# Kernel tuning notes

Hardware: AMD Instinct MI355X
Metric: run time of the kernel (lower is better)

Reference implementation:

```python
import jax, jax.numpy as jnp
from jax import lax
import numpy as np

GRID = 256   # spatial_shape of the sparse voxel volume (D=H=W)
N_ACTIVE = 500000
K = 5        # kernel_size=5, padding=2, stride=1 -> 'same' box-sum conv


def setup_inputs() -> dict:
    key = jax.random.key(0)
    k1, k2 = jax.random.split(key)
    feats = jax.random.normal(k1, (N_ACTIVE,), dtype=jnp.float32)
    coords = jax.random.randint(k2, (N_ACTIVE, 3), 0, GRID, dtype=jnp.int32)
    return {"feats": feats, "coords": coords}


def reference(feats, coords):
    # Densify the sparse tensor: scatter active-voxel features into [B=1, C=1, D, H, W].
    vol = jnp.zeros((1, 1, GRID, GRID, GRID), dtype=feats.dtype)
    vol = vol.at[0, 0, coords[:, 0], coords[:, 1], coords[:, 2]].add(feats)
    # Frozen all-ones 5x5x5 kernel (weight.data = ones, requires_grad=False), no bias.
    kernel = jnp.ones((1, 1, K, K, K), dtype=feats.dtype)  # OIDHW
    pad = K // 2
    out = lax.conv_general_dilated(
        vol, kernel,
        window_strides=(1, 1, 1),
        padding=[(pad, pad)] * 3,
        dimension_numbers=("NCDHW", "OIDHW", "NCDHW"),
    )
    # Original returns a list of one dense volume; return the array.
    return out
```

## Files before the change

### kernel.cpp

```cpp
#include <hip/hip_runtime.h>

#define GRIDN 256
#define NVOX (GRIDN * GRIDN * GRIDN)

typedef float floatx4 __attribute__((ext_vector_type(4)));

__global__ __launch_bounds__(256) void k_prep(const int* __restrict__ coords,
                                              int* __restrict__ lin, int n) {
    int i = blockIdx.x * blockDim.x + threadIdx.x;
    if (i >= n) return;
    int d = coords[3 * i + 0];
    int h = coords[3 * i + 1];
    int w = coords[3 * i + 2];
    lin[i] = (d * GRIDN + h) * GRIDN + w;
}

__global__ __launch_bounds__(256) void k_zero4(floatx4* __restrict__ p, int n4) {
    int stride = gridDim.x * blockDim.x;
    floatx4 z = {0.f, 0.f, 0.f, 0.f};
    for (int i = blockIdx.x * blockDim.x + threadIdx.x; i < n4; i += stride)
        __builtin_nontemporal_store(z, &p[i]);
}

__global__ __launch_bounds__(256) void k_scatter(const float* __restrict__ feats,
                                                 const int* __restrict__ lin,
                                                 float* __restrict__ vol, int n) {
    int i = blockIdx.x * blockDim.x + threadIdx.x;
    if (i >= n) return;
    atomicAdd(&vol[lin[i]], feats[i]);
}

#define TXF 64
#define TYF 16
#define ZS  16
__global__ __launch_bounds__(256) void k_fused(const float4* __restrict__ in4,
                                               float* __restrict__ out) {
    __shared__ float R[TYF + 4][72];
    __shared__ float Xp[TYF + 4][64];

    const int tid = threadIdx.x;

    int wg  = blockIdx.x;
    int swz = (wg & 7) * 128 + (wg >> 3);
    const int x0 = (swz & 3) * TXF;
    const int y0 = ((swz >> 2) & 15) * TYF;
    const int z0 = (swz >> 6) * ZS;

    const int xq = (tid & 15) * 4;
    const int yy = tid >> 4;

    const int i1   = tid + 256;
    const int row0 = tid / 18, c40 = tid - row0 * 18;
    const int row1 = i1 / 18,  c41 = i1 - row1 * 18;
    const int gy0 = y0 + row0 - 2, gx0 = (x0 >> 2) - 1 + c40;
    const int gy1 = y0 + row1 - 2, gx1 = (x0 >> 2) - 1 + c41;
    const bool ok0 = ((unsigned)gy0 < (unsigned)GRIDN) && ((unsigned)gx0 < 64u);
    const bool ok1 = (i1 < 360) && ((unsigned)gy1 < (unsigned)GRIDN) && ((unsigned)gx1 < 64u);
    const int off0 = gy0 * 64 + gx0;
    const int off1 = gy1 * 64 + gx1;

    float4 r0 = {0, 0, 0, 0}, r1 = {0, 0, 0, 0};
    if ((unsigned)(z0 - 2) < (unsigned)GRIDN) {
        const float4* s = in4 + (size_t)(z0 - 2) * (GRIDN * GRIDN / 4);
        if (ok0) r0 = s[off0];
        if (ok1) r1 = s[off1];
    }

    float4 a0 = {0,0,0,0}, a1 = {0,0,0,0}, a2 = {0,0,0,0},
           a3 = {0,0,0,0}, a4 = {0,0,0,0};

    for (int zi = z0 - 2; zi < z0 + ZS + 2; ++zi) {
        *(float4*)&R[row0][c40 * 4] = r0;
        if (i1 < 360) *(float4*)&R[row1][c41 * 4] = r1;
        {
            int zn = zi + 1;
            r0 = make_float4(0.f, 0.f, 0.f, 0.f);
            r1 = make_float4(0.f, 0.f, 0.f, 0.f);
            if (zn < z0 + ZS + 2 && (unsigned)zn < (unsigned)GRIDN) {
                const float4* s = in4 + (size_t)zn * (GRIDN * GRIDN / 4);
                if (ok0) r0 = s[off0];
                if (ok1) r1 = s[off1];
            }
        }
        __syncthreads();
        for (int idx = tid; idx < 20 * 16; idx += 256) {
            int row = idx >> 4;
            int c   = idx & 15;
            float4 v0 = *(const float4*)&R[row][c * 4];
            float4 v1 = *(const float4*)&R[row][c * 4 + 4];
            float4 v2 = *(const float4*)&R[row][c * 4 + 8];
            float s123 = v1.x + v1.y + v1.z;
            float4 o;
            o.x = v0.z + v0.w + s123;
            o.y = v0.w + s123 + v1.w;
            o.z = s123 + v1.w + v2.x;
            o.w = v1.y + v1.z + v1.w + v2.x + v2.y;
            *(float4*)&Xp[row][c * 4] = o;
        }
        __syncthreads();
        float4 q0 = *(const float4*)&Xp[yy + 0][xq];
        float4 q1 = *(const float4*)&Xp[yy + 1][xq];
        float4 q2 = *(const float4*)&Xp[yy + 2][xq];
        float4 q3 = *(const float4*)&Xp[yy + 3][xq];
        float4 q4 = *(const float4*)&Xp[yy + 4][xq];
        float4 v;
        v.x = q0.x + q1.x + q2.x + q3.x + q4.x;
        v.y = q0.y + q1.y + q2.y + q3.y + q4.y;
        v.z = q0.z + q1.z + q2.z + q3.z + q4.z;
        v.w = q0.w + q1.w + q2.w + q3.w + q4.w;
        a0 = a1; a1 = a2; a2 = a3; a3 = a4; a4 = v;
        int zo = zi - 2;
        if (zo >= z0) {
            float4 s;
            s.x = a0.x + a1.x + a2.x + a3.x + a4.x;
            s.y = a0.y + a1.y + a2.y + a3.y + a4.y;
            s.z = a0.z + a1.z + a2.z + a3.z + a4.z;
            s.w = a0.w + a1.w + a2.w + a3.w + a4.w;
            float4* op = (float4*)(out + (size_t)zo * (GRIDN * GRIDN)
                                       + (size_t)(y0 + yy) * GRIDN + x0 + xq);
            *op = s;
        }
    }
}

__global__ void k_scatter125(const float* __restrict__ feats,
                             const int* __restrict__ coords,
                             float* __restrict__ out, int n) {
    int i = blockIdx.x * blockDim.x + threadIdx.x;
    if (i >= n) return;
    int d = coords[3 * i + 0];
    int h = coords[3 * i + 1];
    int w = coords[3 * i + 2];
    float f = feats[i];
    int d0 = max(d - 2, 0), d1 = min(d + 2, GRIDN - 1);
    int h0 = max(h - 2, 0), h1 = min(h + 2, GRIDN - 1);
    int w0 = max(w - 2, 0), w1 = min(w + 2, GRIDN - 1);
    for (int dd = d0; dd <= d1; ++dd)
        for (int hh = h0; hh <= h1; ++hh)
            for (int ww = w0; ww <= w1; ++ww)
                atomicAdd(&out[(dd * GRIDN + hh) * GRIDN + ww], f);
}

extern "C" void kernel_launch(void* const* d_in, const int* in_sizes, int n_in,
                              void* d_out, int out_size, void* d_ws, size_t ws_size,
                              hipStream_t stream) {
    const float* feats  = (const float*)d_in[0];
    const int*   coords = (const int*)d_in[1];
    float*       out    = (float*)d_out;
    int n = in_sizes[0];

    const size_t vol_bytes = (size_t)NVOX * sizeof(float);
    const size_t lin_bytes = (size_t)n * sizeof(int);

    if (ws_size >= vol_bytes + lin_bytes) {
        float* ws  = (float*)d_ws;
        int*   lin = (int*)((char*)d_ws + vol_bytes);
        k_prep<<<(n + 255) / 256, 256, 0, stream>>>(coords, lin, n);
        k_zero4<<<4096, 256, 0, stream>>>((floatx4*)ws, NVOX / 4);
        k_scatter<<<(n + 255) / 256, 256, 0, stream>>>(feats, lin, ws, n);
        k_fused<<<1024, 256, 0, stream>>>((const float4*)ws, out);
    } else {
        k_zero4<<<4096, 256, 0, stream>>>((floatx4*)out, NVOX / 4);
        k_scatter125<<<(n + 255) / 256, 256, 0, stream>>>(feats, coords, out, n);
    }
}
```

Baseline: 86.95 us.

## Replace dense scatter volume with z/y-tile point binning and sparse fused conv

Stops densifying the full 256^3 volume in workspace, which required zeroing, atomically scattering into and rereading a 64MB buffer. Points are instead binned into fixed-capacity buckets keyed by z slice and 16-row y tile. The fused kernel reads only nearby bucket records, applies the x-direction 5-tap sum through LDS atomics into a double-buffered plane, and keeps the y/z running sums. The z tile is halved and the grid doubled, which adds halo rework and LDS atomic contention, and bucket overflow beyond 512 points would silently drop data.

Measured after the change: 90.99 us. 4.7% more time.

```diff
diff --git a/kernel.cpp b/kernel.cpp
--- a/kernel.cpp
+++ b/kernel.cpp
@@ -2,112 +2,92 @@
 
 #define GRIDN 256
 #define NVOX (GRIDN * GRIDN * GRIDN)
+#define NYT  16
+#define NBKT (GRIDN * NYT)
+#define BCAP 512
 
 typedef float floatx4 __attribute__((ext_vector_type(4)));
 
-__global__ __launch_bounds__(256) void k_prep(const int* __restrict__ coords,
-                                              int* __restrict__ lin, int n) {
+__global__ __launch_bounds__(256) void k_bin(const float* __restrict__ feats,
+                                             const int* __restrict__ coords,
+                                             int* __restrict__ cnt,
+                                             int2* __restrict__ rec, int n) {
     int i = blockIdx.x * blockDim.x + threadIdx.x;
     if (i >= n) return;
     int d = coords[3 * i + 0];
     int h = coords[3 * i + 1];
     int w = coords[3 * i + 2];
-    lin[i] = (d * GRIDN + h) * GRIDN + w;
-}
-
-__global__ __launch_bounds__(256) void k_zero4(floatx4* __restrict__ p, int n4) {
-    int stride = gridDim.x * blockDim.x;
-    floatx4 z = {0.f, 0.f, 0.f, 0.f};
-    for (int i = blockIdx.x * blockDim.x + threadIdx.x; i < n4; i += stride)
-        __builtin_nontemporal_store(z, &p[i]);
-}
-
-__global__ __launch_bounds__(256) void k_scatter(const float* __restrict__ feats,
-                                                 const int* __restrict__ lin,
-                                                 float* __restrict__ vol, int n) {
-    int i = blockIdx.x * blockDim.x + threadIdx.x;
-    if (i >= n) return;
-    atomicAdd(&vol[lin[i]], feats[i]);
+    int key = d * NYT + (h >> 4);
+    int slot = atomicAdd(&cnt[key], 1);
+    if (slot < BCAP)
+        rec[(size_t)key * BCAP + slot] = make_int2(w | (h << 8), __float_as_int(feats[i]));
 }
 
 #define TXF 64
 #define TYF 16
-#define ZS  16
-__global__ __launch_bounds__(256) void k_fused(const float4* __restrict__ in4,
-                                               float* __restrict__ out) {
-    __shared__ float R[TYF + 4][72];
-    __shared__ float Xp[TYF + 4][64];
+#define ZS  8
+__global__ __launch_bounds__(256) void k_fused_sparse(const int* __restrict__ cnt,
+                                                      const int2* __restrict__ rec,
+                                                      float* __restrict__ out) {
+    __shared__ float Xp[2][TYF + 4][64];
 
     const int tid = threadIdx.x;
-
     int wg  = blockIdx.x;
-    int swz = (wg & 7) * 128 + (wg >> 3);
+    int swz = (wg & 7) * 256 + (wg >> 3);
     const int x0 = (swz & 3) * TXF;
     const int y0 = ((swz >> 2) & 15) * TYF;
     const int z0 = (swz >> 6) * ZS;
 
     const int xq = (tid & 15) * 4;
     const int yy = tid >> 4;
+    const int yt_lo = max(0, (y0 - 2) >> 4);
+    const int yt_hi = min(NYT - 1, (y0 + TYF + 1) >> 4);
 
-    const int i1   = tid + 256;
-    const int row0 = tid / 18, c40 = tid - row0 * 18;
-    const int row1 = i1 / 18,  c41 = i1 - row1 * 18;
-    const int gy0 = y0 + row0 - 2, gx0 = (x0 >> 2) - 1 + c40;
-    const int gy1 = y0 + row1 - 2, gx1 = (x0 >> 2) - 1 + c41;
-    const bool ok0 = ((unsigned)gy0 < (unsigned)GRIDN) && ((unsigned)gx0 < 64u);
-    const bool ok1 = (i1 < 360) && ((unsigned)gy1 < (unsigned)GRIDN) && ((unsigned)gx1 < 64u);
-    const int off0 = gy0 * 64 + gx0;
-    const int off1 = gy1 * 64 + gx1;
-
-    float4 r0 = {0, 0, 0, 0}, r1 = {0, 0, 0, 0};
-    if ((unsigned)(z0 - 2) < (unsigned)GRIDN) {
-        const float4* s = in4 + (size_t)(z0 - 2) * (GRIDN * GRIDN / 4);
-        if (ok0) r0 = s[off0];
-        if (ok1) r1 = s[off1];
-    }
+    for (int idx = tid; idx < 2 * (TYF + 4) * 16; idx += 256)
+        ((float4*)Xp)[idx] = make_float4(0.f, 0.f, 0.f, 0.f);
 
     float4 a0 = {0,0,0,0}, a1 = {0,0,0,0}, a2 = {0,0,0,0},
            a3 = {0,0,0,0}, a4 = {0,0,0,0};
 
     for (int zi = z0 - 2; zi < z0 + ZS + 2; ++zi) {
-        *(float4*)&R[row0][c40 * 4] = r0;
-        if (i1 < 360) *(float4*)&R[row1][c41 * 4] = r1;
-        {
-            int zn = zi + 1;
-            r0 = make_float4(0.f, 0.f, 0.f, 0.f);
-            r1 = make_float4(0.f, 0.f, 0.f, 0.f);
-            if (zn < z0 + ZS + 2 && (unsigned)zn < (unsigned)GRIDN) {
-                const float4* s = in4 + (size_t)zn * (GRIDN * GRIDN / 4);
-                if (ok0) r0 = s[off0];
-                if (ok1) r1 = s[off1];
+        const int cb = zi & 1;
+        __syncthreads();
+        if ((unsigned)zi < (unsigned)GRIDN) {
+            for (int yt = yt_lo; yt <= yt_hi; ++yt) {
+                int b  = zi * NYT + yt;
+                int nb = min(cnt[b], BCAP);
+                const int2* rb = rec + (size_t)b * BCAP;
+                for (int j = tid; j < nb; j += 256) {
+                    int2 r = rb[j];
+                    int x  = r.x & 255;
+                    int y  = (r.x >> 8) & 255;
+                    int ry = y - y0 + 2;
+                    int cx = x - x0;
+                    if ((unsigned)ry < (unsigned)(TYF + 4) && (unsigned)(cx + 2) < 68u) {
+                        float f = __int_as_float(r.y);
+                        #pragma unroll
+                        for (int dx = -2; dx <= 2; ++dx) {
+                            int cc = cx + dx;
+                            if ((unsigned)cc < 64u)
+                                atomicAdd(&Xp[cb][ry][cc], f);
+                        }
+                    }
+                }
             }
         }
         __syncthreads();
-        for (int idx = tid; idx < 20 * 16; idx += 256) {
-            int row = idx >> 4;
-            int c   = idx & 15;
-            float4 v0 = *(const float4*)&R[row][c * 4];
-            float4 v1 = *(const float4*)&R[row][c * 4 + 4];
-            float4 v2 = *(const float4*)&R[row][c * 4 + 8];
-            float s123 = v1.x + v1.y + v1.z;
-            float4 o;
-            o.x = v0.z + v0.w + s123;
-            o.y = v0.w + s123 + v1.w;
-            o.z = s123 + v1.w + v2.x;
-            o.w = v1.y + v1.z + v1.w + v2.x + v2.y;
-            *(float4*)&Xp[row][c * 4] = o;
-        }
-        __syncthreads();
-        float4 q0 = *(const float4*)&Xp[yy + 0][xq];
-        float4 q1 = *(const float4*)&Xp[yy + 1][xq];
-        float4 q2 = *(const float4*)&Xp[yy + 2][xq];
-        float4 q3 = *(const float4*)&Xp[yy + 3][xq];
-        float4 q4 = *(const float4*)&Xp[yy + 4][xq];
+        float4 q0 = *(const float4*)&Xp[cb][yy + 0][xq];
+        float4 q1 = *(const float4*)&Xp[cb][yy + 1][xq];
+        float4 q2 = *(const float4*)&Xp[cb][yy + 2][xq];
+        float4 q3 = *(const float4*)&Xp[cb][yy + 3][xq];
+        float4 q4 = *(const float4*)&Xp[cb][yy + 4][xq];
         float4 v;
         v.x = q0.x + q1.x + q2.x + q3.x + q4.x;
         v.y = q0.y + q1.y + q2.y + q3.y + q4.y;
         v.z = q0.z + q1.z + q2.z + q3.z + q4.z;
         v.w = q0.w + q1.w + q2.w + q3.w + q4.w;
+        for (int idx = tid; idx < (TYF + 4) * 16; idx += 256)
+            ((float4*)Xp[cb ^ 1])[idx] = make_float4(0.f, 0.f, 0.f, 0.f);
         a0 = a1; a1 = a2; a2 = a3; a3 = a4; a4 = v;
         int zo = zi - 2;
         if (zo >= z0) {
@@ -121,6 +101,13 @@
             *op = s;
         }
     }
+}
+
+__global__ __launch_bounds__(256) void k_zero4(floatx4* __restrict__ p, int n4) {
+    int stride = gridDim.x * blockDim.x;
+    floatx4 z = {0.f, 0.f, 0.f, 0.f};
+    for (int i = blockIdx.x * blockDim.x + threadIdx.x; i < n4; i += stride)
+        __builtin_nontemporal_store(z, &p[i]);
 }
 
 __global__ void k_scatter125(const float* __restrict__ feats,
@@ -149,16 +136,15 @@
     float*       out    = (float*)d_out;
     int n = in_sizes[0];
 
-    const size_t vol_bytes = (size_t)NVOX * sizeof(float);
-    const size_t lin_bytes = (size_t)n * sizeof(int);
+    const size_t cnt_bytes = (size_t)NBKT * sizeof(int);
+    const size_t rec_bytes = (size_t)NBKT * BCAP * sizeof(int2);
 
-    if (ws_size >= vol_bytes + lin_bytes) {
-        float* ws  = (float*)d_ws;
-        int*   lin = (int*)((char*)d_ws + vol_bytes);
-        k_prep<<<(n + 255) / 256, 256, 0, stream>>>(coords, lin, n);
-        k_zero4<<<4096, 256, 0, stream>>>((floatx4*)ws, NVOX / 4);
-        k_scatter<<<(n + 255) / 256, 256, 0, stream>>>(feats, lin, ws, n);
-        k_fused<<<1024, 256, 0, stream>>>((const float4*)ws, out);
+    if (ws_size >= cnt_bytes + rec_bytes) {
+        int*  cnt = (int*)d_ws;
+        int2* rec = (int2*)((char*)d_ws + cnt_bytes);
+        hipMemsetAsync(cnt, 0, cnt_bytes, stream);
+        k_bin<<<(n + 255) / 256, 256, 0, stream>>>(feats, coords, cnt, rec, n);
+        k_fused_sparse<<<2048, 256, 0, stream>>>(cnt, rec, out);
     } else {
         k_zero4<<<4096, 256, 0, stream>>>((floatx4*)out, NVOX / 4);
         k_scatter125<<<(n + 255) / 256, 256, 0, stream>>>(feats, coords, out, n);
```
